# Kernel optimization log

Measured on AMD Instinct MI355X. Metric: run time of the kernel, lower is better.

The kernel has to match this reference:

```python
import jax, jax.numpy as jnp
import numpy as np

M, K, N = 65536, 512, 512
EPS = 1e-05


def setup_inputs() -> dict:
    key = jax.random.key(0)
    k1, k2, k3 = jax.random.split(key, 3)
    x = jax.random.normal(k1, (M, K), dtype=jnp.float32)
    # int8 weight buffer in [-128, 127]
    weight_int8 = jax.random.randint(k2, (N, K), -128, 128, dtype=jnp.int32).astype(jnp.int8)
    # realistic per-output-channel dequant scales (max-abs / 127 of an fp weight)
    weight_scale = jax.random.uniform(k3, (N,), dtype=jnp.float32, minval=0.001, maxval=0.02)
    return {"x": x, "weight_int8": weight_int8, "weight_scale": weight_scale}


def reference(x, weight_int8, weight_scale):
    # dynamic per-tensor quantization of the activation
    x_scale = jnp.maximum(jnp.max(jnp.abs(x)) / 127.0, EPS)
    x_int8 = jnp.clip(jnp.round(x / x_scale), -128, 127).astype(jnp.int8)
    out_int32 = jnp.matmul(x_int8, weight_int8.T, preferred_element_type=jnp.int32)
    # dequantize: per-tensor input scale * per-row weight scale
    out = out_int32.astype(jnp.float32) * (x_scale * weight_scale[None, :])
    return out
```

## Files before the change

### kernel.cpp

```cpp
#include <hip/hip_runtime.h>


#define M_DIM 65536
#define K_DIM 512
#define N_DIM 512
#define EPSF  1e-5f

typedef int int32x4 __attribute__((ext_vector_type(4)));

__global__ void absmax1_kernel(const float* __restrict__ x,
                               float* __restrict__ partials) {
    __shared__ float red[4];
    const float4* x4 = (const float4*)x;
    const int base = blockIdx.x * 2048;
    const int t = threadIdx.x;
    float m = 0.0f;
    #pragma unroll
    for (int j = 0; j < 8; ++j) {
        float4 v = x4[base + j * 256 + t];
        m = fmaxf(m, fmaxf(fmaxf(fabsf(v.x), fabsf(v.y)),
                           fmaxf(fabsf(v.z), fabsf(v.w))));
    }
    #pragma unroll
    for (int off = 32; off > 0; off >>= 1)
        m = fmaxf(m, __shfl_xor(m, off));
    if ((t & 63) == 0) red[t >> 6] = m;
    __syncthreads();
    if (t == 0)
        partials[blockIdx.x] = fmaxf(fmaxf(red[0], red[1]),
                                     fmaxf(red[2], red[3]));
}

__global__ void absmax2_kernel(const float* __restrict__ partials,
                               unsigned int* __restrict__ ws) {
    __shared__ float red[4];
    const int t = threadIdx.x;
    const float4* p4 = (const float4*)partials;
    float m = 0.0f;
    #pragma unroll
    for (int j = 0; j < 4; ++j) {
        float4 v = p4[t + j * 256];
        m = fmaxf(m, fmaxf(fmaxf(v.x, v.y), fmaxf(v.z, v.w)));
    }
    #pragma unroll
    for (int off = 32; off > 0; off >>= 1)
        m = fmaxf(m, __shfl_xor(m, off));
    if ((t & 63) == 0) red[t >> 6] = m;
    __syncthreads();
    if (t == 0) {
        float r = fmaxf(fmaxf(red[0], red[1]), fmaxf(red[2], red[3]));
        ws[0] = __float_as_uint(r);
    }
}

__global__ void pack_kernel(const int* __restrict__ wi,
                            unsigned int* __restrict__ wp, int n4) {
    int i = blockIdx.x * blockDim.x + threadIdx.x;
    if (i < n4) {
        int4 v = ((const int4*)wi)[i];
        wp[i] = (v.x & 0xff) | ((v.y & 0xff) << 8) |
                ((v.z & 0xff) << 16) | ((unsigned)v.w << 24);
    }
}

__device__ inline unsigned int quantpack4(float4 f, float inv) {
    const float C = 12582912.0f;
    unsigned int u0 = __float_as_uint(fmaf(f.x, inv, C));
    unsigned int u1 = __float_as_uint(fmaf(f.y, inv, C));
    unsigned int u2 = __float_as_uint(fmaf(f.z, inv, C));
    unsigned int u3 = __float_as_uint(fmaf(f.w, inv, C));
    unsigned int lo = __builtin_amdgcn_perm(u1, u0, 0x0C0C0400u);
    unsigned int hi = __builtin_amdgcn_perm(u3, u2, 0x04000C0Cu);
    return lo | hi;
}

__global__ __launch_bounds__(256, 2) void gemm_kernel(
    const float* __restrict__ x, const signed char* __restrict__ w,
    const float* __restrict__ wscale, const unsigned int* __restrict__ ws,
    float* __restrict__ out) {
    __shared__ signed char Blds[64 * 1024];

    const int wave = threadIdx.x >> 6;
    const int lane = threadIdx.x & 63;
    const int quad = lane >> 4;
    const int l16  = lane & 15;

    const int id  = blockIdx.x;
    const int xcd = id & 7;
    const int j   = id >> 3;
    const int by  = xcd * 64 + (j >> 2);
    const int bx  = j & 3;
    const int m0 = by * 128;
    const int n0 = bx * 128;

    #pragma unroll
    for (int cc = 0; cc < 2; ++cc) {
        int c = wave * 2 + cc;
        #pragma unroll
        for (int t = 0; t < 8; ++t) {
            const signed char* g = w + (long)(n0 + t * 16 + l16) * K_DIM
                                     + c * 64 + quad * 16;
            __builtin_amdgcn_global_load_lds(
                (const __attribute__((address_space(1))) unsigned int*)g,
                (__attribute__((address_space(3))) unsigned int*)(Blds + (c * 8 + t) * 1024),
                16, 0, 0);
        }
    }

    float mx  = __uint_as_float(ws[0]);
    float s   = fmaxf(mx / 127.0f, EPSF);
    float inv = 1.0f / s;

    const int mw = m0 + wave * 32;
    const float* xr0 = x + (long)(mw + l16) * K_DIM + quad * 16;
    const float* xr1 = xr0 + (long)16 * K_DIM;

    int32x4 acc0[8] = {};
    int32x4 acc1[8] = {};

    __syncthreads();

    #pragma unroll
    for (int k0 = 0; k0 < K_DIM; k0 += 64) {
        const float4* xp0 = (const float4*)(xr0 + k0);
        const float4* xp1 = (const float4*)(xr1 + k0);
        float4 f0 = xp0[0], f1 = xp0[1], f2 = xp0[2], f3 = xp0[3];
        float4 g0 = xp1[0], g1 = xp1[1], g2 = xp1[2], g3 = xp1[3];
        int32x4 a0, a1;
        a0.x = (int)quantpack4(f0, inv);
        a0.y = (int)quantpack4(f1, inv);
        a0.z = (int)quantpack4(f2, inv);
        a0.w = (int)quantpack4(f3, inv);
        a1.x = (int)quantpack4(g0, inv);
        a1.y = (int)quantpack4(g1, inv);
        a1.z = (int)quantpack4(g2, inv);
        a1.w = (int)quantpack4(g3, inv);

        const signed char* bbase = Blds + (k0 >> 6) * 8192 + lane * 16;
        #pragma unroll
        for (int t = 0; t < 8; ++t) {
            int32x4 b = *(const int32x4*)(bbase + t * 1024);
            acc0[t] = __builtin_amdgcn_mfma_i32_16x16x64_i8(a0, b, acc0[t], 0, 0, 0);
            acc1[t] = __builtin_amdgcn_mfma_i32_16x16x64_i8(a1, b, acc1[t], 0, 0, 0);
        }
    }

    #pragma unroll
    for (int t = 0; t < 8; ++t) {
        int n = n0 + t * 16 + l16;
        float c = s * wscale[n];
        float* o0 = out + (long)(mw + quad * 4) * N_DIM + n;
        float* o1 = o0 + (long)16 * N_DIM;
        #pragma unroll
        for (int r = 0; r < 4; ++r) {
            o0[(long)r * N_DIM] = (float)acc0[t][r] * c;
            o1[(long)r * N_DIM] = (float)acc1[t][r] * c;
        }
    }
}

extern "C" void kernel_launch(void* const* d_in, const int* in_sizes, int n_in,
                              void* d_out, int out_size, void* d_ws, size_t ws_size,
                              hipStream_t stream) {
    const float* x   = (const float*)d_in[0];
    const int*   wi  = (const int*)d_in[1];
    const float* sc  = (const float*)d_in[2];
    float*       out = (float*)d_out;

    unsigned int* ws_abs   = (unsigned int*)d_ws;
    float*        partials = (float*)((char*)d_ws + 256);
    unsigned int* wp       = (unsigned int*)((char*)d_ws + 32768);
    const signed char* w8  = (const signed char*)wp;

    absmax1_kernel<<<4096, 256, 0, stream>>>(x, partials);
    absmax2_kernel<<<1, 256, 0, stream>>>(partials, ws_abs);

    const int n4w = (N_DIM * K_DIM) / 4;
    pack_kernel<<<n4w / 256, 256, 0, stream>>>(wi, wp, n4w);

    gemm_kernel<<<2048, 256, 0, stream>>>(x, w8, sc, ws_abs, out);
}
```

Measured before the change: 300.1 us.

## Pre-quantize activations to int8 buffer and fuse absmax with weight packing

Weight packing moves into the first absmax pass as extra blocks, which saves a launch. A new quant kernel redoes the final absmax reduction in every block and writes int8 activations to workspace. The GEMM then reads int8 A instead of fp32 and skips the repeated per-tile quantization. In exchange, x is re-read once and an extra 32 MB int8 buffer is written and read, plus there is a fallback path when the workspace is too small.

```diff
diff --git a/kernel.cpp b/kernel.cpp
--- a/kernel.cpp
+++ b/kernel.cpp
@@ -8,59 +8,14 @@
 
 typedef int int32x4 __attribute__((ext_vector_type(4)));
 
-__global__ void absmax1_kernel(const float* __restrict__ x,
-                               float* __restrict__ partials) {
-    __shared__ float red[4];
-    const float4* x4 = (const float4*)x;
-    const int base = blockIdx.x * 2048;
-    const int t = threadIdx.x;
-    float m = 0.0f;
-    #pragma unroll
-    for (int j = 0; j < 8; ++j) {
-        float4 v = x4[base + j * 256 + t];
-        m = fmaxf(m, fmaxf(fmaxf(fabsf(v.x), fabsf(v.y)),
-                           fmaxf(fabsf(v.z), fabsf(v.w))));
-    }
-    #pragma unroll
-    for (int off = 32; off > 0; off >>= 1)
-        m = fmaxf(m, __shfl_xor(m, off));
-    if ((t & 63) == 0) red[t >> 6] = m;
-    __syncthreads();
-    if (t == 0)
-        partials[blockIdx.x] = fmaxf(fmaxf(red[0], red[1]),
-                                     fmaxf(red[2], red[3]));
-}
-
-__global__ void absmax2_kernel(const float* __restrict__ partials,
-                               unsigned int* __restrict__ ws) {
-    __shared__ float red[4];
-    const int t = threadIdx.x;
-    const float4* p4 = (const float4*)partials;
-    float m = 0.0f;
-    #pragma unroll
-    for (int j = 0; j < 4; ++j) {
-        float4 v = p4[t + j * 256];
-        m = fmaxf(m, fmaxf(fmaxf(v.x, v.y), fmaxf(v.z, v.w)));
-    }
-    #pragma unroll
-    for (int off = 32; off > 0; off >>= 1)
-        m = fmaxf(m, __shfl_xor(m, off));
-    if ((t & 63) == 0) red[t >> 6] = m;
-    __syncthreads();
-    if (t == 0) {
-        float r = fmaxf(fmaxf(red[0], red[1]), fmaxf(red[2], red[3]));
-        ws[0] = __float_as_uint(r);
-    }
-}
-
-__global__ void pack_kernel(const int* __restrict__ wi,
-                            unsigned int* __restrict__ wp, int n4) {
-    int i = blockIdx.x * blockDim.x + threadIdx.x;
-    if (i < n4) {
-        int4 v = ((const int4*)wi)[i];
-        wp[i] = (v.x & 0xff) | ((v.y & 0xff) << 8) |
-                ((v.z & 0xff) << 16) | ((unsigned)v.w << 24);
-    }
+#define WS_PART   256
+#define WS_WPACK  32768
+#define WS_X8     294912
+#define WS_NEEDED ((size_t)WS_X8 + (size_t)M_DIM * K_DIM)
+
+__device__ inline unsigned int pack_w4(int4 v) {
+    return (v.x & 0xff) | ((v.y & 0xff) << 8) |
+           ((v.z & 0xff) << 16) | ((unsigned)v.w << 24);
 }
 
 __device__ inline unsigned int quantpack4(float4 f, float inv) {
@@ -74,7 +29,165 @@
     return lo | hi;
 }
 
-__global__ __launch_bounds__(256, 2) void gemm_kernel(
+__global__ void absmax1_pack_kernel(const float* __restrict__ x,
+                                    const int* __restrict__ wi,
+                                    float* __restrict__ partials,
+                                    unsigned int* __restrict__ wp) {
+    const int b = blockIdx.x;
+    const int t = threadIdx.x;
+    if (b < 4096) {
+        __shared__ float red[4];
+        const float4* x4 = (const float4*)x;
+        const int base = b * 2048;
+        float m = 0.0f;
+        #pragma unroll
+        for (int j = 0; j < 8; ++j) {
+            float4 v = x4[base + j * 256 + t];
+            m = fmaxf(m, fmaxf(fmaxf(fabsf(v.x), fabsf(v.y)),
+                               fmaxf(fabsf(v.z), fabsf(v.w))));
+        }
+        #pragma unroll
+        for (int off = 32; off > 0; off >>= 1)
+            m = fmaxf(m, __shfl_xor(m, off));
+        if ((t & 63) == 0) red[t >> 6] = m;
+        __syncthreads();
+        if (t == 0)
+            partials[b] = fmaxf(fmaxf(red[0], red[1]), fmaxf(red[2], red[3]));
+    } else {
+        const int bb = b - 4096;
+        #pragma unroll
+        for (int j = 0; j < 4; ++j) {
+            int d = bb * 1024 + j * 256 + t;
+            wp[d] = pack_w4(((const int4*)wi)[d]);
+        }
+    }
+}
+
+__global__ void quant_kernel(const float* __restrict__ x,
+                             const float* __restrict__ partials,
+                             unsigned int* __restrict__ ws_abs,
+                             unsigned int* __restrict__ x8) {
+    __shared__ float red[4];
+    const int t = threadIdx.x;
+    const float4* p4 = (const float4*)partials;
+    float m = 0.0f;
+    #pragma unroll
+    for (int j = 0; j < 4; ++j) {
+        float4 v = p4[t + j * 256];
+        m = fmaxf(m, fmaxf(fmaxf(v.x, v.y), fmaxf(v.z, v.w)));
+    }
+    #pragma unroll
+    for (int off = 32; off > 0; off >>= 1)
+        m = fmaxf(m, __shfl_xor(m, off));
+    if ((t & 63) == 0) red[t >> 6] = m;
+    __syncthreads();
+    m = fmaxf(fmaxf(red[0], red[1]), fmaxf(red[2], red[3]));
+    const float s   = fmaxf(m / 127.0f, EPSF);
+    const float inv = 1.0f / s;
+    if (blockIdx.x == 0 && t == 0) ws_abs[0] = __float_as_uint(s);
+
+    const float4* x4 = (const float4*)x;
+    const int base = blockIdx.x * 4096;
+    #pragma unroll
+    for (int j = 0; j < 16; ++j) {
+        int idx = base + j * 256 + t;
+        x8[idx] = quantpack4(x4[idx], inv);
+    }
+}
+
+__global__ void absmax2_kernel(const float* __restrict__ partials,
+                               unsigned int* __restrict__ ws) {
+    __shared__ float red[4];
+    const int t = threadIdx.x;
+    const float4* p4 = (const float4*)partials;
+    float m = 0.0f;
+    #pragma unroll
+    for (int j = 0; j < 4; ++j) {
+        float4 v = p4[t + j * 256];
+        m = fmaxf(m, fmaxf(fmaxf(v.x, v.y), fmaxf(v.z, v.w)));
+    }
+    #pragma unroll
+    for (int off = 32; off > 0; off >>= 1)
+        m = fmaxf(m, __shfl_xor(m, off));
+    if ((t & 63) == 0) red[t >> 6] = m;
+    __syncthreads();
+    if (t == 0)
+        ws[0] = __float_as_uint(fmaxf(fmaxf(red[0], red[1]),
+                                      fmaxf(red[2], red[3])));
+}
+
+__global__ __launch_bounds__(256, 2) void gemm8_kernel(
+    const signed char* __restrict__ x8, const signed char* __restrict__ w,
+    const float* __restrict__ wscale, const unsigned int* __restrict__ ws,
+    float* __restrict__ out) {
+    __shared__ signed char Blds[64 * 1024];
+
+    const int wave = threadIdx.x >> 6;
+    const int lane = threadIdx.x & 63;
+    const int quad = lane >> 4;
+    const int l16  = lane & 15;
+
+    const int id  = blockIdx.x;
+    const int xcd = id & 7;
+    const int j   = id >> 3;
+    const int by  = xcd * 64 + (j >> 2);
+    const int bx  = j & 3;
+    const int m0 = by * 128;
+    const int n0 = bx * 128;
+
+    #pragma unroll
+    for (int cc = 0; cc < 2; ++cc) {
+        int c = wave * 2 + cc;
+        #pragma unroll
+        for (int t = 0; t < 8; ++t) {
+            const signed char* g = w + (long)(n0 + t * 16 + l16) * K_DIM
+                                     + c * 64 + quad * 16;
+            __builtin_amdgcn_global_load_lds(
+                (const __attribute__((address_space(1))) unsigned int*)g,
+                (__attribute__((address_space(3))) unsigned int*)(Blds + (c * 8 + t) * 1024),
+                16, 0, 0);
+        }
+    }
+
+    const float s = __uint_as_float(ws[0]);
+
+    const int mw = m0 + wave * 32;
+    const signed char* xr0 = x8 + (long)(mw + l16) * K_DIM + quad * 16;
+    const signed char* xr1 = xr0 + (long)16 * K_DIM;
+
+    int32x4 acc0[8] = {};
+    int32x4 acc1[8] = {};
+
+    __syncthreads();
+
+    #pragma unroll
+    for (int k0 = 0; k0 < K_DIM; k0 += 64) {
+        int32x4 a0 = *(const int32x4*)(xr0 + k0);
+        int32x4 a1 = *(const int32x4*)(xr1 + k0);
+        const signed char* bbase = Blds + (k0 >> 6) * 8192 + lane * 16;
+        #pragma unroll
+        for (int t = 0; t < 8; ++t) {
+            int32x4 b = *(const int32x4*)(bbase + t * 1024);
+            acc0[t] = __builtin_amdgcn_mfma_i32_16x16x64_i8(a0, b, acc0[t], 0, 0, 0);
+            acc1[t] = __builtin_amdgcn_mfma_i32_16x16x64_i8(a1, b, acc1[t], 0, 0, 0);
+        }
+    }
+
+    #pragma unroll
+    for (int t = 0; t < 8; ++t) {
+        int n = n0 + t * 16 + l16;
+        float c = s * wscale[n];
+        float* o0 = out + (long)(mw + quad * 4) * N_DIM + n;
+        float* o1 = o0 + (long)16 * N_DIM;
+        #pragma unroll
+        for (int r = 0; r < 4; ++r) {
+            o0[(long)r * N_DIM] = (float)acc0[t][r] * c;
+            o1[(long)r * N_DIM] = (float)acc1[t][r] * c;
+        }
+    }
+}
+
+__global__ __launch_bounds__(256, 2) void gemm_f32_kernel(
     const float* __restrict__ x, const signed char* __restrict__ w,
     const float* __restrict__ wscale, const unsigned int* __restrict__ ws,
     float* __restrict__ out) {
@@ -168,15 +281,19 @@
     float*       out = (float*)d_out;
 
     unsigned int* ws_abs   = (unsigned int*)d_ws;
-    float*        partials = (float*)((char*)d_ws + 256);
-    unsigned int* wp       = (unsigned int*)((char*)d_ws + 32768);
+    float*        partials = (float*)((char*)d_ws + WS_PART);
+    unsigned int* wp       = (unsigned int*)((char*)d_ws + WS_WPACK);
+    unsigned int* x8       = (unsigned int*)((char*)d_ws + WS_X8);
     const signed char* w8  = (const signed char*)wp;
 
-    absmax1_kernel<<<4096, 256, 0, stream>>>(x, partials);
-    absmax2_kernel<<<1, 256, 0, stream>>>(partials, ws_abs);
-
-    const int n4w = (N_DIM * K_DIM) / 4;
-    pack_kernel<<<n4w / 256, 256, 0, stream>>>(wi, wp, n4w);
-
-    gemm_kernel<<<2048, 256, 0, stream>>>(x, w8, sc, ws_abs, out);
-}
+    absmax1_pack_kernel<<<4160, 256, 0, stream>>>(x, wi, partials, wp);
+
+    if (ws_size >= WS_NEEDED) {
+        quant_kernel<<<2048, 256, 0, stream>>>(x, partials, ws_abs, x8);
+        gemm8_kernel<<<2048, 256, 0, stream>>>((const signed char*)x8, w8, sc,
+                                               ws_abs, out);
+    } else {
+        absmax2_kernel<<<1, 256, 0, stream>>>(partials, ws_abs);
+        gemm_f32_kernel<<<2048, 256, 0, stream>>>(x, w8, sc, ws_abs, out);
+    }
+}
```

Measured after the change: 282.8 us. 5.8% less time.
